# Performance work log

Measured on AMD Instinct MI355X. Metric: run time of the kernel, lower is better.

The kernel has to match this reference:

```python
import jax, jax.numpy as jnp
import numpy as np

B, H, E, G, SEQ_LEN = 131072, 64, 16, 32, 30


def setup_inputs() -> dict:
    key = jax.random.key(0)
    ks = jax.random.split(key, 17)
    def lin(kw, kb, out_f, in_f):
        s = 1.0 / np.sqrt(in_f)
        W = jax.random.uniform(kw, (out_f, in_f), jnp.float32, -s, s)
        b = jax.random.uniform(kb, (out_f,), jnp.float32, -s, s)
        return W, b
    W_se, b_se = lin(ks[0], ks[1], E, 2)
    W_h2p, b_h2p = lin(ks[2], ks[3], 2, 3 * H)
    W_goal, b_goal = lin(ks[4], ks[5], H, 2 * G)
    W_abs, b_abs = lin(ks[6], ks[7], H, 2)
    W_ih, b_ih = lin(ks[8], ks[9], 4 * H, E)
    W_hh, b_hh = lin(ks[10], ks[11], 4 * H, H)
    return {
        "traj_abs": jax.random.normal(ks[12], (1, B, 2), jnp.float32),
        "traj_rel": jax.random.normal(ks[13], (1, B, 2), jnp.float32),
        "h0": jax.random.normal(ks[14], (1, B, H), jnp.float32),
        "c0": jax.random.normal(ks[15], (1, B, H), jnp.float32),
        "goals": jax.random.normal(ks[16], (B, G, 2), jnp.float32),
        "W_ih": W_ih, "W_hh": W_hh, "b_ih": b_ih, "b_hh": b_hh,
        "W_se": W_se, "b_se": b_se,
        "W_h2p": W_h2p, "b_h2p": b_h2p,
        "W_goal": W_goal, "b_goal": b_goal,
        "W_abs": W_abs, "b_abs": b_abs,
    }


def reference(traj_abs, traj_rel, h0, c0, goals,
              W_ih, W_hh, b_ih, b_hh,
              W_se, b_se, W_h2p, b_h2p,
              W_goal, b_goal, W_abs, b_abs):
    b = traj_abs.shape[1]
    goal_emb = goals.reshape(b, -1) @ W_goal.T + b_goal            # (b, H)
    dec_in = jax.nn.leaky_relu(traj_rel[0] @ W_se.T + b_se)        # (b, E)

    def step(carry, _):
        h, c, x, abs_pos = carry
        gates = x @ W_ih.T + b_ih + h @ W_hh.T + b_hh              # (b, 4H)
        i, f, g, o = jnp.split(gates, 4, axis=-1)                  # PyTorch gate order
        c = jax.nn.sigmoid(f) * c + jax.nn.sigmoid(i) * jnp.tanh(g)
        h = jax.nn.sigmoid(o) * jnp.tanh(c)
        abs_emb = abs_pos @ W_abs.T + b_abs                        # (b, H)
        inp = jnp.concatenate([h, abs_emb, goal_emb], axis=1)      # (b, 3H)
        rel = inp @ W_h2p.T + b_h2p                                # (b, 2)
        x = jax.nn.leaky_relu(rel @ W_se.T + b_se)
        return (h, c, x, abs_pos + rel), rel

    _, rels = jax.lax.scan(step, (h0[0], c0[0], dec_in, traj_abs[0]),
                           None, length=SEQ_LEN)
    return rels  # (seq_len, b, 2)
```

## Files before the change

### kernel.cpp

```cpp
#include <hip/hip_runtime.h>
#include <stdint.h>


#define B_TOT 131072
#define SEQL 30
#define NT 2

typedef _Float16 f16x8 __attribute__((ext_vector_type(8)));
typedef _Float16 f16x2 __attribute__((ext_vector_type(2)));
typedef float f32x4 __attribute__((ext_vector_type(4)));
typedef float f32x2 __attribute__((ext_vector_type(2)));

__device__ __forceinline__ float fexp2(float x) {
#if __has_builtin(__builtin_amdgcn_exp2f)
  return __builtin_amdgcn_exp2f(x);
#else
  return exp2f(x);
#endif
}
__device__ __forceinline__ float frcp(float x) {
#if __has_builtin(__builtin_amdgcn_rcpf)
  return __builtin_amdgcn_rcpf(x);
#else
  return 1.0f / x;
#endif
}

__global__ void setup_consts(const float* __restrict__ Wgoal,
                             const float* __restrict__ bgoal,
                             const float* __restrict__ Wh2p,
                             const float* __restrict__ bh2p,
                             const float* __restrict__ Wabs,
                             const float* __restrict__ babs,
                             float* __restrict__ wsf) {
  const int tid = threadIdx.x;
  const int wv = tid >> 6;
  const int lane = tid & 63;
  if (wv == 0) {
    const int k = lane;
    float s0 = 0.f, s1 = 0.f;
#pragma unroll 8
    for (int jj = 0; jj < 64; ++jj) {
      float wg = Wgoal[jj * 64 + k];
      s0 += wg * Wh2p[128 + jj];
      s1 += wg * Wh2p[320 + jj];
    }
    wsf[k] = s0;
    wsf[64 + k] = s1;
  } else {
    const int i = lane >> 3, sub = lane & 7;
    const int p = i & 1, grp = i >> 1;
    float s = 0.f;
#pragma unroll
    for (int t = 0; t < 8; ++t) {
      int j = sub * 8 + t;
      float wv_ = (grp < 3) ? Wh2p[p * 192 + 64 + j] : Wh2p[p * 192 + 128 + j];
      float av = (grp == 0)   ? Wabs[j * 2 + 0]
                 : (grp == 1) ? Wabs[j * 2 + 1]
                 : (grp == 2) ? babs[j]
                              : bgoal[j];
      s += av * wv_;
    }
    s += __shfl_xor(s, 1, 64);
    s += __shfl_xor(s, 2, 64);
    s += __shfl_xor(s, 4, 64);
    if (sub == 0) {
      if (grp == 2) s += bh2p[p];
      wsf[128 + i] = s;
    }
  }
}

__global__ __launch_bounds__(256, 3) void lstm_mfma(
    const float* __restrict__ tabs, const float* __restrict__ trel,
    const float* __restrict__ h0, const float* __restrict__ c0,
    const float* __restrict__ goals, const float* __restrict__ Wih,
    const float* __restrict__ Whh, const float* __restrict__ bih,
    const float* __restrict__ bhh, const float* __restrict__ Wse,
    const float* __restrict__ bse, const float* __restrict__ Wh2p,
    const float* __restrict__ wsf, float* __restrict__ outp) {
  const int lane = threadIdx.x & 63;
  const int w = threadIdx.x >> 6;
  const int q = lane >> 4;
  const int n = lane & 15;
  const int pm = n & 3;
  const int hs = 16 * w;
  const int bbase = blockIdx.x * (16 * NT);

  __shared__ __align__(16) _Float16 hbuf[2 * NT * 16 * 72];

  const float SI = -1.4426950408889634f;
  const float SG = 2.8853900817779268f;
  const float gsc[4] = {SI, SI, SG, SI};
  f16x8 bw[4][3];
#pragma unroll
  for (int g = 0; g < 4; ++g) {
    const int row = g * 64 + hs + n;
    const float sc = gsc[g];
#pragma unroll
    for (int kk = 0; kk < 2; ++kk)
#pragma unroll
      for (int j = 0; j < 8; ++j)
        bw[g][kk][j] = (_Float16)(sc * Whh[row * 64 + kk * 32 + q * 8 + j]);
    float bfold = 0.f, m20 = 0.f, m21 = 0.f;
#pragma unroll
    for (int k = 0; k < 16; ++k) {
      float wik = Wih[row * 16 + k];
      bfold += bse[k] * wik;
      m20 += Wse[k * 2 + 0] * wik;
      m21 += Wse[k * 2 + 1] * wik;
    }
    float bias = sc * (bih[row] + bhh[row] + 0.505f * bfold);
#pragma unroll
    for (int j = 0; j < 8; ++j) {
      float v;
      if (q < 2)
        v = sc * Wih[row * 16 + q * 8 + j];
      else if (q == 2 && j == 0)
        v = bias;
      else if (q == 2 && j == 1)
        v = sc * 0.505f * m20;
      else if (q == 2 && j == 2)
        v = sc * 0.505f * m21;
      else
        v = 0.f;
      bw[g][2][j] = (_Float16)v;
    }
  }
  f16x8 awp0, awp1;
#pragma unroll
  for (int j = 0; j < 8; ++j) {
    float v0 = (pm < 2) ? Wh2p[pm * 192 + q * 8 + j] : 0.f;
    float v1 = (pm < 2) ? Wh2p[pm * 192 + 32 + q * 8 + j] : 0.f;
    awp0[j] = (_Float16)v0;
    awp1[j] = (_Float16)v1;
  }
  const float Sx0 = wsf[128], Sx1 = wsf[129];
  const float Sy0 = wsf[130], Sy1 = wsf[131];

  f16x2 wsaP[4], wsbP[4], bscP[4];
  const uint32_t xmask = (q < 2) ? 0x7FFF7FFFu : 0xFFFFFFFFu;
#pragma unroll
  for (int jj = 0; jj < 4; ++jj) {
    f16x2 z = f16x2{(_Float16)0.f, (_Float16)0.f};
    if (q < 2) {
      int kx = q * 8 + 2 * jj;
      wsaP[jj] =
          f16x2{(_Float16)(0.495f * Wse[kx * 2 + 0]),
                (_Float16)(0.495f * Wse[kx * 2 + 2])};
      wsbP[jj] =
          f16x2{(_Float16)(0.495f * Wse[kx * 2 + 1]),
                (_Float16)(0.495f * Wse[kx * 2 + 3])};
      bscP[jj] = f16x2{(_Float16)(0.495f * bse[kx]),
                       (_Float16)(0.495f * bse[kx + 1])};
    } else if (q == 2 && jj == 0) {
      wsaP[jj] = f16x2{(_Float16)0.f, (_Float16)1.f};
      wsbP[jj] = z;
      bscP[jj] = f16x2{(_Float16)1.f, (_Float16)0.f};
    } else if (q == 2 && jj == 1) {
      wsaP[jj] = z;
      wsbP[jj] = f16x2{(_Float16)1.f, (_Float16)0.f};
      bscP[jj] = z;
    } else {
      wsaP[jj] = z;
      wsbP[jj] = z;
      bscP[jj] = z;
    }
  }

  auto build_x = [&](float r0f, float r1f) -> f16x8 {
    f16x2 r0h = f16x2{(_Float16)r0f, (_Float16)r0f};
    f16x2 r1h = f16x2{(_Float16)r1f, (_Float16)r1f};
    f16x8 xr;
#pragma unroll
    for (int jj = 0; jj < 4; ++jj) {
      f16x2 t = r0h * wsaP[jj] + (r1h * wsbP[jj] + bscP[jj]);
      uint32_t tu = __builtin_bit_cast(uint32_t, t) & xmask;
      f16x2 lr = __builtin_bit_cast(f16x2, tu);
      xr[2 * jj] = lr[0];
      xr[2 * jj + 1] = lr[1];
    }
    return xr;
  };

  const f32x4 zC = {0.f, 0.f, 0.f, 0.f};

  float Gg0[NT], Gg1[NT];
  float ax[NT], ay[NT], cst[NT][4];
  f16x8 xf[NT];
  {
    f16x8 aM0, aM1;
#pragma unroll
    for (int j = 0; j < 8; ++j) {
      int k = q * 8 + j;
      aM0[j] = (_Float16)((pm < 2) ? wsf[pm * 64 + k] : 0.f);
      aM1[j] = (_Float16)((pm < 2) ? wsf[pm * 64 + 32 + k] : 0.f);
    }
    const float Sb0 = wsf[132] + wsf[134];
    const float Sb1 = wsf[133] + wsf[135];
#pragma unroll
    for (int t = 0; t < NT; ++t) {
      const int bb = bbase + 16 * t;
      f16x8 bg0, bg1;
#pragma unroll
      for (int j = 0; j < 8; ++j) {
        int k = q * 8 + j;
        bg0[j] = (_Float16)goals[(bb + n) * 64 + k];
        bg1[j] = (_Float16)goals[(bb + n) * 64 + 32 + k];
      }
      f32x4 Ga = __builtin_amdgcn_mfma_f32_16x16x32_f16(aM0, bg0, zC, 0, 0, 0);
      Ga = __builtin_amdgcn_mfma_f32_16x16x32_f16(aM1, bg1, Ga, 0, 0, 0);
      Gg0[t] = Ga[0] + Sb0;
      Gg1[t] = Ga[1] + Sb1;

      ax[t] = tabs[(bb + n) * 2 + 0];
      ay[t] = tabs[(bb + n) * 2 + 1];
#pragma unroll
      for (int r = 0; r < 4; ++r) {
        const int b = bb + 4 * q + r;
        cst[t][r] = c0[b * 64 + hs + n];
        hbuf[t * 1152 + (4 * q + r) * 72 + hs + n] =
            (_Float16)h0[b * 64 + hs + n];
      }
      xf[t] = build_x(trel[(bb + n) * 2 + 0], trel[(bb + n) * 2 + 1]);
    }
  }

  const int ro = n * 72 + q * 8;
  const int wo = (4 * q) * 72 + hs + n;
  const float K2 = 2.8853900817779268f;

  int poff = 0;
  for (int s = 0; s <= SEQL; ++s) {
    __syncthreads();
    f16x8 ah0[NT], ah1[NT];
#pragma unroll
    for (int t = 0; t < NT; ++t) {
      ah0[t] = *(const f16x8*)(hbuf + poff + t * 1152 + ro);
      ah1[t] = *(const f16x8*)(hbuf + poff + t * 1152 + ro + 32);
    }

    if (s > 0) {
#pragma unroll
      for (int t = 0; t < NT; ++t) {
        f32x4 p = __builtin_amdgcn_mfma_f32_16x16x32_f16(awp0, ah0[t], zC,
                                                         0, 0, 0);
        p = __builtin_amdgcn_mfma_f32_16x16x32_f16(awp1, ah1[t], p, 0, 0, 0);
        float u0 = p[0] + Gg0[t] + fmaf(ax[t], Sx0, ay[t] * Sy0);
        float u1 = p[1] + Gg1[t] + fmaf(ax[t], Sx1, ay[t] * Sy1);
        ax[t] += u0;
        ay[t] += u1;
        if (w == t && lane < 16) {
          float2 v;
          v.x = u0;
          v.y = u1;
          ((float2*)outp)[(size_t)(s - 1) * B_TOT + bbase + 16 * t + lane] = v;
        }
        xf[t] = build_x(u0, u1);
      }
    }

    if (s < SEQL) {
      f32x4 acc[NT][4];
#pragma unroll
      for (int g = 0; g < 4; ++g)
#pragma unroll
        for (int t = 0; t < NT; ++t) {
          f32x4 a = __builtin_amdgcn_mfma_f32_16x16x32_f16(ah0[t], bw[g][0],
                                                           zC, 0, 0, 0);
          a = __builtin_amdgcn_mfma_f32_16x16x32_f16(ah1[t], bw[g][1], a,
                                                     0, 0, 0);
          a = __builtin_amdgcn_mfma_f32_16x16x32_f16(xf[t], bw[g][2], a,
                                                     0, 0, 0);
          acc[t][g] = a;
        }
#pragma unroll
      for (int t = 0; t < NT; ++t) {
        _Float16* hw = hbuf + (poff ^ 2304) + t * 1152 + wo;
#pragma unroll
        for (int pr = 0; pr < 2; ++pr) {
          const int ra = 2 * pr, rb = 2 * pr + 1;
          f32x2 Av = {fexp2(acc[t][0][ra]), fexp2(acc[t][0][rb])};
          f32x2 Fv = {fexp2(acc[t][1][ra]), fexp2(acc[t][1][rb])};
          f32x2 Bv = {fexp2(acc[t][2][ra]), fexp2(acc[t][2][rb])};
          const f32x2 one = {1.f, 1.f};
          f32x2 t1 = Av + one;
          f32x2 t2 = Bv + one;
          f32x2 t3 = Fv + one;
          f32x2 t4 = Bv - one;
          f32x2 m1 = t1 * t2;
          f32x2 cs = {cst[t][ra], cst[t][rb]};
          f32x2 num = cs * m1 + t4 * t3;
          f32x2 den = m1 * t3;
          f32x2 cc = {num[0] * frcp(den[0]), num[1] * frcp(den[1])};
          cst[t][ra] = cc[0];
          cst[t][rb] = cc[1];
          f32x2 Cv = {fexp2(acc[t][3][ra]), fexp2(acc[t][3][rb])};
          f32x2 k2c = cc * K2;
          f32x2 Dv = {fexp2(k2c[0]), fexp2(k2c[1])};
          f32x2 hd = (Cv + one) * (Dv + one);
          f32x2 hnm = Dv - one;
          hw[72 * ra] = (_Float16)(hnm[0] * frcp(hd[0]));
          hw[72 * rb] = (_Float16)(hnm[1] * frcp(hd[1]));
        }
      }
      poff ^= 2304;
    }
  }
}

extern "C" void kernel_launch(void* const* d_in, const int* in_sizes, int n_in,
                              void* d_out, int out_size, void* d_ws,
                              size_t ws_size, hipStream_t stream) {
  (void)in_sizes; (void)n_in; (void)out_size; (void)ws_size;
  const float* tabs  = (const float*)d_in[0];
  const float* trel  = (const float*)d_in[1];
  const float* h0    = (const float*)d_in[2];
  const float* c0    = (const float*)d_in[3];
  const float* goals = (const float*)d_in[4];
  const float* Wih   = (const float*)d_in[5];
  const float* Whh   = (const float*)d_in[6];
  const float* bih   = (const float*)d_in[7];
  const float* bhh   = (const float*)d_in[8];
  const float* Wse   = (const float*)d_in[9];
  const float* bse   = (const float*)d_in[10];
  const float* Wh2p  = (const float*)d_in[11];
  const float* bh2p  = (const float*)d_in[12];
  const float* Wgoal = (const float*)d_in[13];
  const float* bgoal = (const float*)d_in[14];
  const float* Wabs  = (const float*)d_in[15];
  const float* babs  = (const float*)d_in[16];
  float* wsf = (float*)d_ws;

  setup_consts<<<dim3(1), dim3(128), 0, stream>>>(Wgoal, bgoal, Wh2p, bh2p,
                                                  Wabs, babs, wsf);
  lstm_mfma<<<dim3(B_TOT / (16 * NT)), dim3(256), 0, stream>>>(
      tabs, trel, h0, c0, goals, Wih, Whh, bih, bhh, Wse, bse, Wh2p, wsf,
      (float*)d_out);
}
```

Before: 462.6 us.

## Process four batch tiles per block in pairs and share reciprocals

Each block now handles four 16-row batch tiles instead of two, with occupancy lowered from 3 to 2 blocks per SM. Tiles are processed in pairs to keep register pressure bounded. The double-buffer offset is widened to match. Pairs of reciprocals in the gate math are merged into one reciprocal plus extra multiplies, which cuts transcendental-unit work but risks overflow when the two denominators are multiplied together.

```diff
diff --git a/kernel.cpp b/kernel.cpp
--- a/kernel.cpp
+++ b/kernel.cpp
@@ -4,7 +4,7 @@
 
 #define B_TOT 131072
 #define SEQL 30
-#define NT 2
+#define NT 4
 
 typedef _Float16 f16x8 __attribute__((ext_vector_type(8)));
 typedef _Float16 f16x2 __attribute__((ext_vector_type(2)));
@@ -71,7 +71,7 @@
   }
 }
 
-__global__ __launch_bounds__(256, 3) void lstm_mfma(
+__global__ __launch_bounds__(256, 2) void lstm_mfma(
     const float* __restrict__ tabs, const float* __restrict__ trel,
     const float* __restrict__ h0, const float* __restrict__ c0,
     const float* __restrict__ goals, const float* __restrict__ Wih,
@@ -233,79 +233,90 @@
   int poff = 0;
   for (int s = 0; s <= SEQL; ++s) {
     __syncthreads();
-    f16x8 ah0[NT], ah1[NT];
-#pragma unroll
-    for (int t = 0; t < NT; ++t) {
-      ah0[t] = *(const f16x8*)(hbuf + poff + t * 1152 + ro);
-      ah1[t] = *(const f16x8*)(hbuf + poff + t * 1152 + ro + 32);
-    }
-
-    if (s > 0) {
-#pragma unroll
-      for (int t = 0; t < NT; ++t) {
-        f32x4 p = __builtin_amdgcn_mfma_f32_16x16x32_f16(awp0, ah0[t], zC,
-                                                         0, 0, 0);
-        p = __builtin_amdgcn_mfma_f32_16x16x32_f16(awp1, ah1[t], p, 0, 0, 0);
-        float u0 = p[0] + Gg0[t] + fmaf(ax[t], Sx0, ay[t] * Sy0);
-        float u1 = p[1] + Gg1[t] + fmaf(ax[t], Sx1, ay[t] * Sy1);
-        ax[t] += u0;
-        ay[t] += u1;
-        if (w == t && lane < 16) {
-          float2 v;
-          v.x = u0;
-          v.y = u1;
-          ((float2*)outp)[(size_t)(s - 1) * B_TOT + bbase + 16 * t + lane] = v;
+
+#pragma unroll
+    for (int p2 = 0; p2 < NT / 2; ++p2) {
+      f16x8 ah0[2], ah1[2];
+#pragma unroll
+      for (int u = 0; u < 2; ++u) {
+        const int t = 2 * p2 + u;
+        ah0[u] = *(const f16x8*)(hbuf + poff + t * 1152 + ro);
+        ah1[u] = *(const f16x8*)(hbuf + poff + t * 1152 + ro + 32);
+      }
+
+      if (s > 0) {
+#pragma unroll
+        for (int u = 0; u < 2; ++u) {
+          const int t = 2 * p2 + u;
+          f32x4 p = __builtin_amdgcn_mfma_f32_16x16x32_f16(awp0, ah0[u], zC,
+                                                           0, 0, 0);
+          p = __builtin_amdgcn_mfma_f32_16x16x32_f16(awp1, ah1[u], p, 0, 0, 0);
+          float u0 = p[0] + Gg0[t] + fmaf(ax[t], Sx0, ay[t] * Sy0);
+          float u1 = p[1] + Gg1[t] + fmaf(ax[t], Sx1, ay[t] * Sy1);
+          ax[t] += u0;
+          ay[t] += u1;
+          if (w == t && lane < 16) {
+            float2 v;
+            v.x = u0;
+            v.y = u1;
+            ((float2*)outp)[(size_t)(s - 1) * B_TOT + bbase + 16 * t + lane] =
+                v;
+          }
+          xf[t] = build_x(u0, u1);
         }
-        xf[t] = build_x(u0, u1);
-      }
-    }
-
-    if (s < SEQL) {
-      f32x4 acc[NT][4];
-#pragma unroll
-      for (int g = 0; g < 4; ++g)
-#pragma unroll
-        for (int t = 0; t < NT; ++t) {
-          f32x4 a = __builtin_amdgcn_mfma_f32_16x16x32_f16(ah0[t], bw[g][0],
-                                                           zC, 0, 0, 0);
-          a = __builtin_amdgcn_mfma_f32_16x16x32_f16(ah1[t], bw[g][1], a,
-                                                     0, 0, 0);
-          a = __builtin_amdgcn_mfma_f32_16x16x32_f16(xf[t], bw[g][2], a,
-                                                     0, 0, 0);
-          acc[t][g] = a;
+      }
+
+      if (s < SEQL) {
+        f32x4 acc[2][4];
+#pragma unroll
+        for (int g = 0; g < 4; ++g)
+#pragma unroll
+          for (int u = 0; u < 2; ++u) {
+            const int t = 2 * p2 + u;
+            f32x4 a = __builtin_amdgcn_mfma_f32_16x16x32_f16(ah0[u], bw[g][0],
+                                                             zC, 0, 0, 0);
+            a = __builtin_amdgcn_mfma_f32_16x16x32_f16(ah1[u], bw[g][1], a,
+                                                       0, 0, 0);
+            a = __builtin_amdgcn_mfma_f32_16x16x32_f16(xf[t], bw[g][2], a,
+                                                       0, 0, 0);
+            acc[u][g] = a;
+          }
+#pragma unroll
+        for (int u = 0; u < 2; ++u) {
+          const int t = 2 * p2 + u;
+          _Float16* hw = hbuf + (poff ^ 4608) + t * 1152 + wo;
+#pragma unroll
+          for (int pr = 0; pr < 2; ++pr) {
+            const int ra = 2 * pr, rb = 2 * pr + 1;
+            f32x2 Av = {fexp2(acc[u][0][ra]), fexp2(acc[u][0][rb])};
+            f32x2 Fv = {fexp2(acc[u][1][ra]), fexp2(acc[u][1][rb])};
+            f32x2 Bv = {fexp2(acc[u][2][ra]), fexp2(acc[u][2][rb])};
+            const f32x2 one = {1.f, 1.f};
+            f32x2 t1 = Av + one;
+            f32x2 t2 = Bv + one;
+            f32x2 t3 = Fv + one;
+            f32x2 t4 = Bv - one;
+            f32x2 m1 = t1 * t2;
+            f32x2 cs = {cst[t][ra], cst[t][rb]};
+            f32x2 num = cs * m1 + t4 * t3;
+            f32x2 den = m1 * t3;
+            float Rc = frcp(den[0] * den[1]);
+            float cc0 = num[0] * den[1] * Rc;
+            float cc1 = num[1] * den[0] * Rc;
+            cst[t][ra] = cc0;
+            cst[t][rb] = cc1;
+            f32x2 Cv = {fexp2(acc[u][3][ra]), fexp2(acc[u][3][rb])};
+            f32x2 Dv = {fexp2(K2 * cc0), fexp2(K2 * cc1)};
+            f32x2 hd = (Cv + one) * (Dv + one);
+            f32x2 hnm = Dv - one;
+            float Rh = frcp(hd[0] * hd[1]);
+            hw[72 * ra] = (_Float16)(hnm[0] * hd[1] * Rh);
+            hw[72 * rb] = (_Float16)(hnm[1] * hd[0] * Rh);
+          }
         }
-#pragma unroll
-      for (int t = 0; t < NT; ++t) {
-        _Float16* hw = hbuf + (poff ^ 2304) + t * 1152 + wo;
-#pragma unroll
-        for (int pr = 0; pr < 2; ++pr) {
-          const int ra = 2 * pr, rb = 2 * pr + 1;
-          f32x2 Av = {fexp2(acc[t][0][ra]), fexp2(acc[t][0][rb])};
-          f32x2 Fv = {fexp2(acc[t][1][ra]), fexp2(acc[t][1][rb])};
-          f32x2 Bv = {fexp2(acc[t][2][ra]), fexp2(acc[t][2][rb])};
-          const f32x2 one = {1.f, 1.f};
-          f32x2 t1 = Av + one;
-          f32x2 t2 = Bv + one;
-          f32x2 t3 = Fv + one;
-          f32x2 t4 = Bv - one;
-          f32x2 m1 = t1 * t2;
-          f32x2 cs = {cst[t][ra], cst[t][rb]};
-          f32x2 num = cs * m1 + t4 * t3;
-          f32x2 den = m1 * t3;
-          f32x2 cc = {num[0] * frcp(den[0]), num[1] * frcp(den[1])};
-          cst[t][ra] = cc[0];
-          cst[t][rb] = cc[1];
-          f32x2 Cv = {fexp2(acc[t][3][ra]), fexp2(acc[t][3][rb])};
-          f32x2 k2c = cc * K2;
-          f32x2 Dv = {fexp2(k2c[0]), fexp2(k2c[1])};
-          f32x2 hd = (Cv + one) * (Dv + one);
-          f32x2 hnm = Dv - one;
-          hw[72 * ra] = (_Float16)(hnm[0] * frcp(hd[0]));
-          hw[72 * rb] = (_Float16)(hnm[1] * frcp(hd[1]));
-        }
-      }
-      poff ^= 2304;
-    }
+      }
+    }
+    if (s < SEQL) poff ^= 4608;
   }
 }
 
```

Result: no change. 468.1 us (+1.2%).
